# Kernel optimization log

Hardware: AMD Instinct MI355X
Metric: run time of the kernel (lower is better)

## Reference

```python
import jax, jax.numpy as jnp
import numpy as np

B, N, C = 16, 25200, 80      # batch, anchors (YOLOv5@640), COCO classes
T_MAX = 50                   # max targets per image
MAX_DET = 300                # NMS candidate cap (static output size)
CONF_THRES = 0.8
NMS_THRES = 0.4


def cxcywh_to_xyxy(b):
    # cxcywh -> xywh -> xyxy, as in tensor_to_dict
    cx, cy, w, h = b[..., 0], b[..., 1], b[..., 2], b[..., 3]
    half_w, half_h = w * 0.5, h * 0.5
    return jnp.stack([cx - half_w, cy - half_h, cx + half_w, cy + half_h], axis=-1)


def iou_matrix(b):
    # b: [K,4] xyxy -> [K,K] pairwise IoU
    area = (b[:, 2] - b[:, 0]) * (b[:, 3] - b[:, 1])
    lt = jnp.maximum(b[:, None, :2], b[None, :, :2])
    rb = jnp.minimum(b[:, None, 2:], b[None, :, 2:])
    wh = jnp.clip(rb - lt, 0.0)
    inter = wh[..., 0] * wh[..., 1]
    return inter / (area[:, None] + area[None, :] - inter + 1e-9)


def nms_keep(boxes, valid):
    # boxes sorted by score desc; greedy NMS -> bool keep mask [K]
    K = boxes.shape[0]
    iou = iou_matrix(boxes)
    idx = jnp.arange(K)

    def body(i, keep):
        k = keep[i]  # survivor & valid
        suppress = k & (iou[i] > NMS_THRES) & (idx > i)
        return keep & ~suppress

    return jax.lax.fori_loop(0, K, body, valid)


def post_process(logits):
    # logits: [B, N, 4+1+C]
    boxes = cxcywh_to_xyxy(logits[..., :4])          # [B,N,4]
    obj = logits[..., 4]                             # [B,N]
    cls = logits[..., 5:]                            # [B,N,C]
    cls_conf = jnp.max(cls, axis=-1)
    labels = jnp.argmax(cls, axis=-1)
    conf = obj * cls_conf                            # [B,N]
    score = jnp.where(conf > CONF_THRES, conf, -jnp.inf)
    top_s, top_i = jax.lax.top_k(score, MAX_DET)     # [B,K]
    bb = jnp.take_along_axis(boxes, top_i[..., None], axis=1)   # [B,K,4]
    lb = jnp.take_along_axis(labels, top_i, axis=1)             # [B,K]
    valid = top_s > CONF_THRES
    scores = jnp.where(valid, top_s, 0.0)
    keep = jax.vmap(nms_keep)(bb, valid)             # [B,K]
    return bb, scores, lb.astype(jnp.int32), keep


def setup_inputs() -> dict:
    key = jax.random.key(0)
    k1, k2, k3 = jax.random.split(key, 3)
    logits = jax.random.uniform(k1, (B, N, 5 + C), dtype=jnp.float32)
    targets = jax.random.uniform(k2, (B, T_MAX, 6), dtype=jnp.float32)
    target_lengths = jax.random.randint(k3, (B,), 1, T_MAX, dtype=jnp.int64)
    return {"logits": logits, "targets": targets, "target_lengths": target_lengths}


def reference(logits, targets, target_lengths):
    pred_boxes, pred_scores, pred_labels, pred_keep = post_process(logits)
    # targets: ragged slice expressed as a validity mask (jit-static shapes)
    tgt_valid = jnp.arange(T_MAX)[None, :] < target_lengths[:, None]   # [B,T]
    tgt_boxes = cxcywh_to_xyxy(targets[..., :4])                       # [B,T,4]
    tgt_scores = targets[..., 4]
    tgt_labels = targets[..., 5].astype(jnp.int32)                     # labels.shape[1]==1 branch
    return (pred_boxes, pred_scores, pred_labels, pred_keep,
            tgt_boxes, tgt_scores, tgt_labels, tgt_valid)
```

## Files before the change

### kernel.cpp

```cpp
#include <hip/hip_runtime.h>
#include <stdint.h>

#define BATCH   16
#define NANCH   25200
#define NCLS    80
#define REC     85
#define MAXDET  300
#define TMAX    50
#define NBUCKET 2048
#define FIN     512
#define SUPW    3008

#define OFF_PB 0
#define OFF_PS 19200
#define OFF_PL 24000
#define OFF_PK 28800
#define OFF_TB 33600
#define OFF_TS 36800
#define OFF_TL 37600
#define OFF_TV 38400

__device__ __forceinline__ float opaque_f(float x) { asm volatile("" : "+v"(x)); return x; }

__global__ __launch_bounds__(256) void kA(const float* __restrict__ logits,
                                          unsigned* __restrict__ confout,
                                          unsigned* __restrict__ labout) {
    const int wid  = (blockIdx.x * 256 + threadIdx.x) >> 6;
    const int lane = threadIdx.x & 63;
    const int t    = lane >> 2;
    const int j    = lane & 3;
    const int a    = wid * 16 + t;
    const float obj = logits[(size_t)a * REC + 4];
    unsigned cf = 0u;
    if (obj > 0.8f) {
        const float* cls = logits + (size_t)a * REC + 5 + j * 20;
        float v[20];
#pragma unroll
        for (int i = 0; i < 5; ++i) {
            float4 q = *(const float4*)(cls + 4 * i);
            v[4*i+0] = q.x; v[4*i+1] = q.y; v[4*i+2] = q.z; v[4*i+3] = q.w;
        }
        float m = v[0];
#pragma unroll
        for (int i = 1; i < 20; ++i) m = fmaxf(m, v[i]);
        m = fmaxf(m, __shfl_xor(m, 1));
        m = fmaxf(m, __shfl_xor(m, 2));
        int lc = 255;
#pragma unroll
        for (int i = 0; i < 20; ++i) lc = min(lc, (v[i] == m) ? (j * 20 + i) : 255);
        lc = min(lc, __shfl_xor(lc, 1));
        lc = min(lc, __shfl_xor(lc, 2));
        const float conf = obj * m;
        cf = (conf > 0.8f) ? __float_as_uint(conf) : 0u;
        if (j == 0) labout[a] = (unsigned)lc;
    }
    if (j == 0) confout[a] = cf;
}

__global__ __launch_bounds__(1024) void kSel(const float* __restrict__ logits,
                                             const unsigned* __restrict__ confbits,
                                             const unsigned* __restrict__ labels,
                                             const float* __restrict__ targets,
                                             const int* __restrict__ tlen,
                                             float* __restrict__ out) {
    __shared__ unsigned hist[NBUCKET];
    __shared__ unsigned long long fin[FIN];
    __shared__ unsigned long long srt[MAXDET];
    __shared__ int sTb, sCnt;
    const int b = blockIdx.x;
    const int tid = threadIdx.x;
    const int lane = tid & 63;

    if (tid >= 512 && tid < 512 + TMAX) {
        int t = tid - 512;
        bool is64 = (tlen[1] == 0) && (tlen[3] == 0) && (tlen[5] == 0);
        int len = is64 ? tlen[2 * b] : tlen[b];
        const float* r = targets + ((size_t)b * TMAX + t) * 6;
        float cx = r[0], cy = r[1], w = r[2], h = r[3], sc = r[4], lb = r[5];
        float hw = opaque_f(w * 0.5f);
        float hh = opaque_f(h * 0.5f);
        size_t o = (size_t)b * TMAX + t;
        out[OFF_TB + o * 4 + 0] = cx - hw;
        out[OFF_TB + o * 4 + 1] = cy - hh;
        out[OFF_TB + o * 4 + 2] = cx + hw;
        out[OFF_TB + o * 4 + 3] = cy + hh;
        out[OFF_TS + o] = sc;
        out[OFF_TL + o] = (float)(int)lb;
        out[OFF_TV + o] = (t < len) ? 1.0f : 0.0f;
    }

    for (int i = tid; i < NBUCKET; i += 1024) hist[i] = 0u;
    if (tid < MAXDET) srt[tid] = 0ull;
    if (tid == 0) sCnt = 0;
    __syncthreads();

    const unsigned* cb = confbits + (size_t)b * NANCH;
    const uint4* cb4 = (const uint4*)cb;
    for (int i = tid; i < NANCH / 4; i += 1024) {
        uint4 u = cb4[i];
        unsigned w0 = u.x, w1 = u.y, w2 = u.z, w3 = u.w;
        if (w0) { unsigned bk = (w0 - 0x3F4CCCCDu) >> 11; if (bk > NBUCKET-1u) bk = NBUCKET-1u; atomicAdd(&hist[bk], 1u); }
        if (w1) { unsigned bk = (w1 - 0x3F4CCCCDu) >> 11; if (bk > NBUCKET-1u) bk = NBUCKET-1u; atomicAdd(&hist[bk], 1u); }
        if (w2) { unsigned bk = (w2 - 0x3F4CCCCDu) >> 11; if (bk > NBUCKET-1u) bk = NBUCKET-1u; atomicAdd(&hist[bk], 1u); }
        if (w3) { unsigned bk = (w3 - 0x3F4CCCCDu) >> 11; if (bk > NBUCKET-1u) bk = NBUCKET-1u; atomicAdd(&hist[bk], 1u); }
    }
    __syncthreads();

    if (tid < 64) {
        const int l = tid;
        unsigned sup = 0u;
        for (int j = 0; j < 32; ++j) sup += hist[l * 32 + j];
        unsigned ss = sup;
        for (int off = 1; off < 64; off <<= 1) {
            unsigned v = __shfl_down(ss, off);
            ss += (l + off < 64) ? v : 0u;
        }
        bool ge = ss >= MAXDET;
        unsigned long long mask = __ballot(ge);
        int sstar = (mask == 0ull) ? 0 : (63 - __clzll(mask));
        unsigned tail = (sstar < 63) ? __shfl(ss, sstar + 1) : 0u;
        unsigned h = (l < 32) ? hist[sstar * 32 + l] : 0u;
        unsigned s2 = h;
        for (int off = 1; off < 32; off <<= 1) {
            unsigned v = __shfl_down(s2, off);
            s2 += (l + off < 32) ? v : 0u;
        }
        bool ge2 = (l < 32) && (s2 + tail >= MAXDET);
        unsigned long long m2 = __ballot(ge2);
        int lstar = (m2 == 0ull) ? 0 : (63 - __clzll(m2));
        if (l == 0) sTb = sstar * 32 + lstar;
    }
    __syncthreads();

    const int tb = sTb;
    for (int i = tid; i < NANCH / 4; i += 1024) {
        uint4 u = cb4[i];
        unsigned wsv[4] = {u.x, u.y, u.z, u.w};
#pragma unroll
        for (int c = 0; c < 4; ++c) {
            unsigned bits = wsv[c];
            unsigned bk = (bits - 0x3F4CCCCDu) >> 11;
            if (bk > NBUCKET - 1u) bk = NBUCKET - 1u;
            bool pass = bits && ((int)bk >= tb);
            unsigned long long mk = __ballot(pass);
            if (mk) {
                int base = 0;
                if (lane == 0) base = atomicAdd(&sCnt, __popcll(mk));
                base = __shfl(base, 0);
                if (pass) {
                    int p = base + __popcll(mk & ((1ull << lane) - 1ull));
                    if (p < FIN)
                        fin[p] = ((unsigned long long)bits << 32) |
                                 (unsigned)(0xFFFFFFFFu - (unsigned)(i * 4 + c));
                }
            }
        }
    }
    __syncthreads();
    const int fc = (sCnt < FIN) ? sCnt : FIN;

    if (tid < fc) {
        unsigned long long k = fin[tid];
        int r = 0;
        for (int j = 0; j < fc; ++j) r += (fin[j] > k) ? 1 : 0;
        if (r < MAXDET) srt[r] = k;
    }
    __syncthreads();

    if (tid < MAXDET) {
        unsigned long long key = srt[tid];
        float score = __uint_as_float((unsigned)(key >> 32));
        unsigned n = 0xFFFFFFFFu - (unsigned)(key & 0xFFFFFFFFull);
        if (n >= NANCH) n = 0;
        const size_t ga = (size_t)b * NANCH + n;
        float4 bq = *(const float4*)(logits + ga * REC);
        unsigned lab = labels[ga];
        float hw = opaque_f(bq.z * 0.5f);
        float hh = opaque_f(bq.w * 0.5f);
        float x1 = bq.x - hw, y1 = bq.y - hh, x2 = bq.x + hw, y2 = bq.y + hh;
        size_t o = (size_t)(b * MAXDET + tid);
        out[OFF_PB + o * 4 + 0] = x1;
        out[OFF_PB + o * 4 + 1] = y1;
        out[OFF_PB + o * 4 + 2] = x2;
        out[OFF_PB + o * 4 + 3] = y2;
        out[OFF_PS + o] = score;
        out[OFF_PL + o] = (float)lab;
    }
}

__global__ __launch_bounds__(256) void kSup(const float* __restrict__ out,
                                            unsigned* __restrict__ suppg) {
    __shared__ float4 sb[MAXDET];
    __shared__ float sar[MAXDET];
    const int b = blockIdx.x >> 3;
    const int s = blockIdx.x & 7;
    const int tid = threadIdx.x;
    const int lane = tid & 63;
    const int w = tid >> 6;
    const float4* boxes = (const float4*)(out + OFF_PB) + (size_t)b * MAXDET;
    for (int t = tid; t < MAXDET; t += 256) {
        float4 q = boxes[t];
        sb[t] = q;
        sar[t] = (q.z - q.x) * (q.w - q.y);
    }
    __syncthreads();
    const int i0 = s * 38;
    const int i1 = min(i0 + 38, MAXDET);
    unsigned* sg = suppg + (size_t)b * SUPW;
    for (int i = i0 + w; i < i1; i += 4) {
        float4 bi = sb[i];
        float ai = sar[i];
#pragma unroll
        for (int c = 0; c < 5; ++c) {
            int j = c * 64 + lane;
            bool pass = false;
            if (j < MAXDET && j > i) {
                float4 bj = sb[j];
                float aj = sar[j];
                float ltx = fmaxf(bi.x, bj.x);
                float lty = fmaxf(bi.y, bj.y);
                float rbx = fminf(bi.z, bj.z);
                float rby = fminf(bi.w, bj.w);
                float wx = fmaxf(rbx - ltx, 0.0f);
                float wy = fmaxf(rby - lty, 0.0f);
                float inter = wx * wy;
                float iou = inter / (ai + aj - inter + 1e-9f);
                pass = (iou > 0.4f);
            }
            unsigned long long mk = __ballot(pass);
            if (lane == 0)  sg[i * 10 + 2 * c]     = (unsigned)mk;
            if (lane == 32) sg[i * 10 + 2 * c + 1] = (unsigned)(mk >> 32);
        }
    }
}

__global__ __launch_bounds__(512) void kScan(const unsigned* __restrict__ suppg,
                                             float* __restrict__ out) {
    __shared__ unsigned supp[MAXDET * 10];
    __shared__ unsigned keepw[10];
    const int b = blockIdx.x;
    const int tid = threadIdx.x;
    const unsigned* sg = suppg + (size_t)b * SUPW;
    for (int t = tid; t < MAXDET * 10; t += 512) supp[t] = sg[t];
    __syncthreads();
    if (tid < 64) {
        int q = tid;
        unsigned kw = (q < 10) ? ((q == 9) ? 0xFFFu : 0xFFFFFFFFu) : 0u;
        unsigned nextrow = (q < 10) ? supp[q] : 0u;
        for (int i = 0; i < MAXDET; ++i) {
            unsigned rowq = nextrow;
            if (q < 10 && i + 1 < MAXDET) nextrow = supp[(i + 1) * 10 + q];
            bool mybit = (q == (i >> 5)) && ((kw >> (i & 31)) & 1u);
            if (__ballot(mybit)) kw &= ~rowq;
        }
        if (q < 10) keepw[q] = kw;
    }
    __syncthreads();
    if (tid < MAXDET)
        out[OFF_PK + (size_t)b * MAXDET + tid] =
            ((keepw[tid >> 5] >> (tid & 31)) & 1u) ? 1.0f : 0.0f;
}

extern "C" void kernel_launch(void* const* d_in, const int* in_sizes, int n_in,
                              void* d_out, int out_size, void* d_ws, size_t ws_size,
                              hipStream_t stream) {
    const float* logits  = (const float*)d_in[0];
    const float* targets = (const float*)d_in[1];
    const int*   tlen    = (const int*)d_in[2];
    float* out = (float*)d_out;
    char* ws = (char*)d_ws;
    unsigned* confbits = (unsigned*)ws;
    unsigned* labels   = (unsigned*)(ws + (size_t)BATCH * NANCH * 4);
    unsigned* suppg    = (unsigned*)(ws + (size_t)BATCH * NANCH * 8);

    hipLaunchKernelGGL(kA, dim3(6300), dim3(256), 0, stream, logits, confbits, labels);
    hipLaunchKernelGGL(kSel, dim3(BATCH), dim3(1024), 0, stream,
                       logits, confbits, labels, targets, tlen, out);
    hipLaunchKernelGGL(kSup, dim3(BATCH * 8), dim3(256), 0, stream, out, suppg);
    hipLaunchKernelGGL(kScan, dim3(BATCH), dim3(512), 0, stream, suppg, out);
}
```

Measured before the change: 72.23 us.

## Build score histogram in the scoring pass and split candidate compaction across blocks

The per-image histogram moves into the first scoring kernel through global atomics, so the selection kernel no longer rereads the confidence array to build it. Threshold finding and candidate compaction now run in a new kernel that uses 8 blocks per image, each compacting one slice into a fixed-capacity per-slice buffer. A final kernel then concatenates the slices and ranks them. This raises parallelism from 16 blocks to 128 for the scan-heavy stage, but it adds a memset, one extra launch, global atomic contention, and a per-slice cap of 96 candidates that could overflow on skewed inputs.

```diff
diff --git a/kernel.cpp b/kernel.cpp
--- a/kernel.cpp
+++ b/kernel.cpp
@@ -8,7 +8,8 @@
 #define MAXDET  300
 #define TMAX    50
 #define NBUCKET 2048
-#define FIN     512
+#define SCAP    96
+#define FINC    768
 #define SUPW    3008
 
 #define OFF_PB 0
@@ -24,7 +25,8 @@
 
 __global__ __launch_bounds__(256) void kA(const float* __restrict__ logits,
                                           unsigned* __restrict__ confout,
-                                          unsigned* __restrict__ labout) {
+                                          unsigned* __restrict__ labout,
+                                          unsigned* __restrict__ histg) {
     const int wid  = (blockIdx.x * 256 + threadIdx.x) >> 6;
     const int lane = threadIdx.x & 63;
     const int t    = lane >> 2;
@@ -54,22 +56,99 @@
         cf = (conf > 0.8f) ? __float_as_uint(conf) : 0u;
         if (j == 0) labout[a] = (unsigned)lc;
     }
-    if (j == 0) confout[a] = cf;
-}
-
-__global__ __launch_bounds__(1024) void kSel(const float* __restrict__ logits,
-                                             const unsigned* __restrict__ confbits,
+    if (j == 0) {
+        confout[a] = cf;
+        if (cf) {
+            int b = a / NANCH;
+            unsigned bk = (cf - 0x3F4CCCCDu) >> 11;
+            if (bk > NBUCKET - 1u) bk = NBUCKET - 1u;
+            atomicAdd(&histg[b * NBUCKET + bk], 1u);
+        }
+    }
+}
+
+__global__ __launch_bounds__(256) void kCmp(const unsigned* __restrict__ confbits,
+                                            const unsigned* __restrict__ histg,
+                                            unsigned long long* __restrict__ fing,
+                                            int* __restrict__ cntg) {
+    __shared__ unsigned hist[NBUCKET];
+    __shared__ int sTb, sCnt;
+    const int b = blockIdx.x >> 3;
+    const int s = blockIdx.x & 7;
+    const int tid = threadIdx.x;
+    const int lane = tid & 63;
+    for (int i = tid; i < NBUCKET; i += 256) hist[i] = histg[b * NBUCKET + i];
+    if (tid == 0) sCnt = 0;
+    __syncthreads();
+    if (tid < 64) {
+        const int l = tid;
+        unsigned sup = 0u;
+        for (int j = 0; j < 32; ++j) sup += hist[l * 32 + j];
+        unsigned ss = sup;
+        for (int off = 1; off < 64; off <<= 1) {
+            unsigned v = __shfl_down(ss, off);
+            ss += (l + off < 64) ? v : 0u;
+        }
+        bool ge = ss >= MAXDET;
+        unsigned long long mask = __ballot(ge);
+        int sstar = (mask == 0ull) ? 0 : (63 - __clzll(mask));
+        unsigned tail = (sstar < 63) ? __shfl(ss, sstar + 1) : 0u;
+        unsigned h = (l < 32) ? hist[sstar * 32 + l] : 0u;
+        unsigned s2 = h;
+        for (int off = 1; off < 32; off <<= 1) {
+            unsigned v = __shfl_down(s2, off);
+            s2 += (l + off < 32) ? v : 0u;
+        }
+        bool ge2 = (l < 32) && (s2 + tail >= MAXDET);
+        unsigned long long m2 = __ballot(ge2);
+        int lstar = (m2 == 0ull) ? 0 : (63 - __clzll(m2));
+        if (l == 0) sTb = sstar * 32 + lstar;
+    }
+    __syncthreads();
+    const int tb = sTb;
+    const uint4* cb4 = (const uint4*)(confbits + (size_t)b * NANCH);
+    const int u40 = s * 788;
+    const int u41 = min(6300, u40 + 788);
+    unsigned long long* fg = fing + (size_t)b * FINC + s * SCAP;
+    for (int i = u40 + tid; i < u41; i += 256) {
+        uint4 u = cb4[i];
+        unsigned wsv[4] = {u.x, u.y, u.z, u.w};
+#pragma unroll
+        for (int c = 0; c < 4; ++c) {
+            unsigned bits = wsv[c];
+            unsigned bk = (bits - 0x3F4CCCCDu) >> 11;
+            if (bk > NBUCKET - 1u) bk = NBUCKET - 1u;
+            bool pass = bits && ((int)bk >= tb);
+            unsigned long long mk = __ballot(pass);
+            if (mk) {
+                int base = 0;
+                if (lane == 0) base = atomicAdd(&sCnt, __popcll(mk));
+                base = __shfl(base, 0);
+                if (pass) {
+                    int p = base + __popcll(mk & ((1ull << lane) - 1ull));
+                    if (p < SCAP)
+                        fg[p] = ((unsigned long long)bits << 32) |
+                                (unsigned)(0xFFFFFFFFu - (unsigned)(i * 4 + c));
+                }
+            }
+        }
+    }
+    __syncthreads();
+    if (tid == 0) cntg[b * 8 + s] = (sCnt < SCAP) ? sCnt : SCAP;
+}
+
+__global__ __launch_bounds__(1024) void kFin(const float* __restrict__ logits,
                                              const unsigned* __restrict__ labels,
+                                             const unsigned long long* __restrict__ fing,
+                                             const int* __restrict__ cntg,
                                              const float* __restrict__ targets,
                                              const int* __restrict__ tlen,
                                              float* __restrict__ out) {
-    __shared__ unsigned hist[NBUCKET];
-    __shared__ unsigned long long fin[FIN];
+    __shared__ unsigned long long fin[FINC];
     __shared__ unsigned long long srt[MAXDET];
-    __shared__ int sTb, sCnt;
+    __shared__ int offs[9];
     const int b = blockIdx.x;
     const int tid = threadIdx.x;
-    const int lane = tid & 63;
 
     if (tid >= 512 && tid < 512 + TMAX) {
         int t = tid - 512;
@@ -89,75 +168,20 @@
         out[OFF_TV + o] = (t < len) ? 1.0f : 0.0f;
     }
 
-    for (int i = tid; i < NBUCKET; i += 1024) hist[i] = 0u;
+    if (tid == 0) {
+        int acc = 0;
+        offs[0] = 0;
+        for (int s = 0; s < 8; ++s) { acc += cntg[b * 8 + s]; offs[s + 1] = acc; }
+    }
     if (tid < MAXDET) srt[tid] = 0ull;
-    if (tid == 0) sCnt = 0;
-    __syncthreads();
-
-    const unsigned* cb = confbits + (size_t)b * NANCH;
-    const uint4* cb4 = (const uint4*)cb;
-    for (int i = tid; i < NANCH / 4; i += 1024) {
-        uint4 u = cb4[i];
-        unsigned w0 = u.x, w1 = u.y, w2 = u.z, w3 = u.w;
-        if (w0) { unsigned bk = (w0 - 0x3F4CCCCDu) >> 11; if (bk > NBUCKET-1u) bk = NBUCKET-1u; atomicAdd(&hist[bk], 1u); }
-        if (w1) { unsigned bk = (w1 - 0x3F4CCCCDu) >> 11; if (bk > NBUCKET-1u) bk = NBUCKET-1u; atomicAdd(&hist[bk], 1u); }
-        if (w2) { unsigned bk = (w2 - 0x3F4CCCCDu) >> 11; if (bk > NBUCKET-1u) bk = NBUCKET-1u; atomicAdd(&hist[bk], 1u); }
-        if (w3) { unsigned bk = (w3 - 0x3F4CCCCDu) >> 11; if (bk > NBUCKET-1u) bk = NBUCKET-1u; atomicAdd(&hist[bk], 1u); }
-    }
-    __syncthreads();
-
-    if (tid < 64) {
-        const int l = tid;
-        unsigned sup = 0u;
-        for (int j = 0; j < 32; ++j) sup += hist[l * 32 + j];
-        unsigned ss = sup;
-        for (int off = 1; off < 64; off <<= 1) {
-            unsigned v = __shfl_down(ss, off);
-            ss += (l + off < 64) ? v : 0u;
-        }
-        bool ge = ss >= MAXDET;
-        unsigned long long mask = __ballot(ge);
-        int sstar = (mask == 0ull) ? 0 : (63 - __clzll(mask));
-        unsigned tail = (sstar < 63) ? __shfl(ss, sstar + 1) : 0u;
-        unsigned h = (l < 32) ? hist[sstar * 32 + l] : 0u;
-        unsigned s2 = h;
-        for (int off = 1; off < 32; off <<= 1) {
-            unsigned v = __shfl_down(s2, off);
-            s2 += (l + off < 32) ? v : 0u;
-        }
-        bool ge2 = (l < 32) && (s2 + tail >= MAXDET);
-        unsigned long long m2 = __ballot(ge2);
-        int lstar = (m2 == 0ull) ? 0 : (63 - __clzll(m2));
-        if (l == 0) sTb = sstar * 32 + lstar;
-    }
-    __syncthreads();
-
-    const int tb = sTb;
-    for (int i = tid; i < NANCH / 4; i += 1024) {
-        uint4 u = cb4[i];
-        unsigned wsv[4] = {u.x, u.y, u.z, u.w};
-#pragma unroll
-        for (int c = 0; c < 4; ++c) {
-            unsigned bits = wsv[c];
-            unsigned bk = (bits - 0x3F4CCCCDu) >> 11;
-            if (bk > NBUCKET - 1u) bk = NBUCKET - 1u;
-            bool pass = bits && ((int)bk >= tb);
-            unsigned long long mk = __ballot(pass);
-            if (mk) {
-                int base = 0;
-                if (lane == 0) base = atomicAdd(&sCnt, __popcll(mk));
-                base = __shfl(base, 0);
-                if (pass) {
-                    int p = base + __popcll(mk & ((1ull << lane) - 1ull));
-                    if (p < FIN)
-                        fin[p] = ((unsigned long long)bits << 32) |
-                                 (unsigned)(0xFFFFFFFFu - (unsigned)(i * 4 + c));
-                }
-            }
-        }
-    }
-    __syncthreads();
-    const int fc = (sCnt < FIN) ? sCnt : FIN;
+    __syncthreads();
+    for (int s = 0; s < 8; ++s) {
+        int o0 = offs[s], c = offs[s + 1] - o0;
+        for (int i = tid; i < c; i += 1024)
+            fin[o0 + i] = fing[(size_t)b * FINC + s * SCAP + i];
+    }
+    __syncthreads();
+    const int fc = offs[8];
 
     if (tid < fc) {
         unsigned long long k = fin[tid];
@@ -270,12 +294,20 @@
     float* out = (float*)d_out;
     char* ws = (char*)d_ws;
     unsigned* confbits = (unsigned*)ws;
-    unsigned* labels   = (unsigned*)(ws + (size_t)BATCH * NANCH * 4);
-    unsigned* suppg    = (unsigned*)(ws + (size_t)BATCH * NANCH * 8);
-
-    hipLaunchKernelGGL(kA, dim3(6300), dim3(256), 0, stream, logits, confbits, labels);
-    hipLaunchKernelGGL(kSel, dim3(BATCH), dim3(1024), 0, stream,
-                       logits, confbits, labels, targets, tlen, out);
-    hipLaunchKernelGGL(kSup, dim3(BATCH * 8), dim3(256), 0, stream, out, suppg);
+    unsigned* labels   = (unsigned*)(ws + 1612800);
+    unsigned* histg    = (unsigned*)(ws + 3225600);
+    int*      cntg     = (int*)     (ws + 3225600 + 131072);
+    unsigned long long* fing =
+        (unsigned long long*)(ws + 3225600 + 131072 + 512);
+    unsigned* suppg    = (unsigned*)(ws + 3225600 + 131072 + 512 + 98304);
+
+    hipMemsetAsync(histg, 0, 131072, stream);
+    hipLaunchKernelGGL(kA,    dim3(6300), dim3(256), 0, stream,
+                       logits, confbits, labels, histg);
+    hipLaunchKernelGGL(kCmp,  dim3(BATCH * 8), dim3(256), 0, stream,
+                       confbits, histg, fing, cntg);
+    hipLaunchKernelGGL(kFin,  dim3(BATCH), dim3(1024), 0, stream,
+                       logits, labels, fing, cntg, targets, tlen, out);
+    hipLaunchKernelGGL(kSup,  dim3(BATCH * 8), dim3(256), 0, stream, out, suppg);
     hipLaunchKernelGGL(kScan, dim3(BATCH), dim3(512), 0, stream, suppg, out);
 }
```

Result: slower. 79.51 us (+10.1%).
